# Optimization experiments

Measured on AMD Instinct MI355X. Metric: run time of the kernel, lower is better.

Reference implementation:

```python
import jax, jax.numpy as jnp
import numpy as np

B, S, D = 4, 2048, 1024
NEG = -1e10

def setup_inputs() -> dict:
    key = jax.random.key(0)
    ks = jax.random.split(key, 8)
    scale = 1.0 / np.sqrt(D)
    return {
        "hidden_states": jax.random.normal(ks[0], (B, S, D), jnp.float32),
        "mask": jax.random.randint(ks[1], (B, S), 0, 2, jnp.int32),
        "Wq": jax.random.normal(ks[2], (D, D), jnp.float32) * scale,
        "bq": jnp.zeros((D,), jnp.float32),
        "Wk": jax.random.normal(ks[3], (D, D), jnp.float32) * scale,
        "bk": jnp.zeros((D,), jnp.float32),
        "Wv": jax.random.normal(ks[4], (D, D), jnp.float32) * scale,
        "bv": jnp.zeros((D,), jnp.float32),
        "Wo": jax.random.normal(ks[5], (D, D), jnp.float32) * scale,
        "bo": jnp.zeros((D,), jnp.float32),
    }

def reference(hidden_states, mask, Wq, bq, Wk, bk, Wv, bv, Wo, bo):
    # torch Linear: y = x @ W.T + b
    q = jnp.einsum('bsd,ed->bse', hidden_states, Wq) + bq
    k = jnp.einsum('bsd,ed->bse', hidden_states, Wk) + bk
    v = jnp.einsum('bsd,ed->bse', hidden_states, Wv) + bv
    inv_sqrt_d = jnp.asarray(int(hidden_states.shape[-1]) ** (-0.5), hidden_states.dtype)
    weight = jnp.einsum('bqd,bkd->bqk', q, k) * inv_sqrt_d  # [B,S,S]
    # mask viewed as [B,1,S]: key-padding mask broadcast over query dim
    m = mask.reshape(mask.shape[0], 1, mask.shape[1])
    weight = jnp.where(m == 0, jnp.asarray(NEG, weight.dtype), weight)
    a = jax.nn.softmax(weight, axis=-1)
    hid = jnp.einsum('bqk,bkd->bqd', a, v)
    hid_o = jnp.einsum('bsd,ed->bse', hid, Wo) + bo
    return hidden_states + hid_o  # residual=True
```

## Files before the change

kernel.cpp:

```cpp
#include <hip/hip_runtime.h>
#include <stdint.h>


typedef __attribute__((ext_vector_type(8))) short bf16x8;
typedef __attribute__((ext_vector_type(4))) float f32x4;

typedef __attribute__((address_space(3))) void lds_void_t;
typedef __attribute__((address_space(1))) const void glb_void_t;

__device__ __forceinline__ ushort f2bf(float f) {
  uint32_t u = __float_as_uint(f);
  u += 0x7FFF + ((u >> 16) & 1);
  return (ushort)(u >> 16);
}
__device__ __forceinline__ float bf2f(ushort u) {
  return __uint_as_float(((uint32_t)u) << 16);
}

__global__ __launch_bounds__(256) void convert_all(
    const float* __restrict__ X, const float* __restrict__ Wq,
    const float* __restrict__ Wk, const float* __restrict__ Wv,
    const float* __restrict__ Wo, const float* __restrict__ bq,
    const float* __restrict__ bk, const float* __restrict__ bv,
    ushort* __restrict__ Xb, ushort* __restrict__ Wqkvb,
    ushort* __restrict__ Wob, float* __restrict__ bqkv) {
  if (blockIdx.x >= 12288) {
#pragma unroll
    for (int u = 0; u < 3; ++u) {
      int base = (u * 256 + threadIdx.x) * 4;
      float4 v = (base < 1024)   ? *(const float4*)(bq + base)
               : (base < 2048)   ? *(const float4*)(bk + base - 1024)
                                 : *(const float4*)(bv + base - 2048);
      *(float4*)(bqkv + base) = v;
    }
    return;
  }
  int64_t o4 = ((int64_t)blockIdx.x * blockDim.x + threadIdx.x) * 4;
  const float* s; ushort* d; int64_t doff, soff;
  if (o4 < 8388608)        { s = X;  d = Xb;    doff = o4;            soff = o4; }
  else if (o4 < 9437184)   { s = Wq; d = Wqkvb; doff = o4 - 8388608;  soff = o4 - 8388608; }
  else if (o4 < 10485760)  { s = Wk; d = Wqkvb; doff = o4 - 8388608;  soff = o4 - 9437184; }
  else if (o4 < 11534336)  { s = Wv; d = Wqkvb; doff = o4 - 8388608;  soff = o4 - 10485760; }
  else                     { s = Wo; d = Wob;   doff = o4 - 11534336; soff = o4 - 11534336; }
  float4 v = *(const float4*)(s + soff);
  ushort4 o;
  o.x = f2bf(v.x); o.y = f2bf(v.y); o.z = f2bf(v.z); o.w = f2bf(v.w);
  *(ushort4*)(d + doff) = o;
}

#define BM 128
#define BKT 64

template <int MODE, int BNV, int GM>
__global__ __launch_bounds__(256) void gemm_bt(
    const ushort* __restrict__ Ag, const ushort* __restrict__ Bg,
    void* __restrict__ Og, const float* __restrict__ bias,
    const float* __restrict__ resid, ushort* __restrict__ Vt,
    const int* __restrict__ maskg, float* __restrict__ rowsum,
    int M, int N, int K, int lda, int ldb, int ldo,
    long long sAz, long long sBz, long long sOz, float scale) {
  constexpr int NFR = BNV / 32;
  __shared__ ushort LDSu[BM * BKT + BNV * BKT];
  ushort* const As = LDSu;
  ushort* const Bs = LDSu + BM * BKT;
  __shared__ int redn[4];

  const int z = blockIdx.z;
  const ushort* A = Ag + (int64_t)z * sAz;
  const ushort* B = Bg + (int64_t)z * sBz;

  const int tilesN = N / BNV;
  const int q8 = gridDim.x >> 3;
  const int wg = (blockIdx.x & 7) * q8 + (blockIdx.x >> 3);
  const int grpSz = GM * tilesN;
  const int tm = (wg / grpSz) * GM + (wg % GM);
  const int tn = (wg % grpSz) / GM;
  const int tid = threadIdx.x;
  const int wid = tid >> 6;
  const int lane = tid & 63;
  const int lr = lane & 15;
  const int kq = lane >> 4;
  const int wr = (wid >> 1) * 64;
  const int wc = (wid & 1) * (BNV / 2);

  if constexpr (MODE == 6) {
    const int4* mrow = (const int4*)(maskg + z * 2048);
    int4 ma = mrow[tid * 2];
    int4 mb = mrow[tid * 2 + 1];
    int cnt = (ma.x == 0) + (ma.y == 0) + (ma.z == 0) + (ma.w == 0) +
              (mb.x == 0) + (mb.y == 0) + (mb.z == 0) + (mb.w == 0);
#pragma unroll
    for (int off = 1; off < 64; off <<= 1) cnt += __shfl_xor(cnt, off);
    if (lane == 0) redn[wid] = cnt;
  }

  f32x4 acc[4][NFR];
#pragma unroll
  for (int m = 0; m < 4; ++m)
#pragma unroll
    for (int n = 0; n < NFR; ++n) acc[m][n] = (f32x4){0.f, 0.f, 0.f, 0.f};

  const int64_t abase = (int64_t)tm * BM;
  const int64_t bbase = (int64_t)tn * BNV;

  for (int kt = 0; kt < K; kt += BKT) {
    if (kt) __syncthreads();
#pragma unroll
    for (int r = 0; r < 4; ++r) {
      int idx = r * 256 + tid;
      int row = idx >> 3, slot = idx & 7;
      int sslot = slot ^ (row & 7);
      const ushort* ga = A + (abase + row) * lda + kt + sslot * 8;
      ushort* la = &As[(r * 256 + wid * 64) * 8];
      __builtin_amdgcn_global_load_lds((glb_void_t*)ga, (lds_void_t*)la, 16, 0, 0);
    }
#pragma unroll
    for (int r = 0; r < BNV / 32; ++r) {
      int idx = r * 256 + tid;
      int row = idx >> 3, slot = idx & 7;
      int sslot = slot ^ (row & 7);
      const ushort* gb = B + (bbase + row) * ldb + kt + sslot * 8;
      ushort* lb = &Bs[(r * 256 + wid * 64) * 8];
      __builtin_amdgcn_global_load_lds((glb_void_t*)gb, (lds_void_t*)lb, 16, 0, 0);
    }
    __syncthreads();

#pragma unroll
    for (int kk = 0; kk < 2; ++kk) {
      bf16x8 af[4], bfr[NFR];
#pragma unroll
      for (int m = 0; m < 4; ++m) {
        int row = wr + m * 16 + lr;
        int slot = (kk * 4 + kq) ^ (row & 7);
        af[m] = *(const bf16x8*)&As[row * 64 + slot * 8];
      }
#pragma unroll
      for (int n = 0; n < NFR; ++n) {
        int col = wc + n * 16 + lr;
        int slot = (kk * 4 + kq) ^ (col & 7);
        bfr[n] = *(const bf16x8*)&Bs[col * 64 + slot * 8];
      }
#pragma unroll
      for (int m = 0; m < 4; ++m)
#pragma unroll
        for (int n = 0; n < NFR; ++n)
          acc[m][n] = __builtin_amdgcn_mfma_f32_16x16x32_bf16(af[m], bfr[n], acc[m][n], 0, 0, 0);
    }
  }

  if constexpr (MODE == 5) {
    float part[4][4];
#pragma unroll
    for (int m = 0; m < 4; ++m)
#pragma unroll
      for (int i = 0; i < 4; ++i) part[m][i] = 0.f;
#pragma unroll
    for (int m = 0; m < 4; ++m) {
      int r0 = tm * BM + wr + m * 16 + kq * 4;
#pragma unroll
      for (int n = 0; n < NFR; ++n) {
        int c = tn * BNV + wc + n * 16 + lr;
#pragma unroll
        for (int i = 0; i < 4; ++i) {
          float e = __expf(acc[m][n][i]);
          ((ushort*)Og)[(int64_t)z * sOz + (int64_t)(r0 + i) * ldo + c] = f2bf(e);
          part[m][i] += e;
        }
      }
    }
#pragma unroll
    for (int off = 1; off <= 8; off <<= 1)
#pragma unroll
      for (int m = 0; m < 4; ++m)
#pragma unroll
        for (int i = 0; i < 4; ++i)
          part[m][i] += __shfl_xor(part[m][i], off);
    if (lr == 0) {
#pragma unroll
      for (int m = 0; m < 4; ++m)
#pragma unroll
        for (int i = 0; i < 4; ++i)
          atomicAdd(&rowsum[z * 2048 + tm * BM + wr + m * 16 + kq * 4 + i],
                    part[m][i]);
    }
  } else if constexpr (MODE == 6) {
    float nm = (float)(redn[0] + redn[1] + redn[2] + redn[3]);
    float invr[4][4];
#pragma unroll
    for (int m = 0; m < 4; ++m)
#pragma unroll
      for (int i = 0; i < 4; ++i)
        invr[m][i] =
            1.0f / (rowsum[z * 2048 + tm * BM + wr + m * 16 + kq * 4 + i] - nm);
#pragma unroll
    for (int m = 0; m < 4; ++m) {
      int r0 = tm * BM + wr + m * 16 + kq * 4;
#pragma unroll
      for (int n = 0; n < NFR; ++n) {
        int c = tn * BNV + wc + n * 16 + lr;
#pragma unroll
        for (int i = 0; i < 4; ++i)
          ((ushort*)Og)[(int64_t)z * sOz + (int64_t)(r0 + i) * ldo + c] =
              f2bf(acc[m][n][i] * invr[m][i]);
      }
    }
  } else if constexpr (MODE == 4) {
    if (tn < 8) {
#pragma unroll
      for (int m = 0; m < 4; ++m) {
        int r0 = tm * BM + wr + m * 16 + kq * 4;
#pragma unroll
        for (int n = 0; n < NFR; ++n) {
          int c = tn * BNV + wc + n * 16 + lr;
          const float bb = bias[c];
#pragma unroll
          for (int i = 0; i < 4; ++i)
            ((ushort*)Og)[(int64_t)(r0 + i) * 2048 + c] =
                f2bf((acc[m][n][i] + bb) * 0.03125f);
        }
      }
    } else if (tn < 16) {
#pragma unroll
      for (int m = 0; m < 4; ++m) {
        int r0 = tm * BM + wr + m * 16 + kq * 4;
        int4 mv = *(const int4*)(maskg + r0);
        int mk[4] = {mv.x, mv.y, mv.z, mv.w};
#pragma unroll
        for (int n = 0; n < NFR; ++n) {
          int c = tn * BNV + wc + n * 16 + lr;
          const float bb = bias[c];
#pragma unroll
          for (int i = 0; i < 4; ++i)
            ((ushort*)Og)[(int64_t)(r0 + i) * 2048 + c] =
                mk[i] ? f2bf(acc[m][n][i] + bb) : (ushort)0;
        }
      }
    } else {
      __syncthreads();
#pragma unroll
      for (int m = 0; m < 4; ++m) {
        int rl0 = wr + m * 16 + kq * 4;
        int4 mv = *(const int4*)(maskg + tm * BM + rl0);
        int mk[4] = {mv.x, mv.y, mv.z, mv.w};
#pragma unroll
        for (int n = 0; n < NFR; ++n) {
          int cl = wc + n * 16 + lr;
          const float bb = bias[tn * BNV + cl];
#pragma unroll
          for (int i = 0; i < 4; ++i) {
            int rl = rl0 + i;
            ushort v = mk[i] ? f2bf(acc[m][n][i] + bb) : (ushort)0;
            LDSu[cl * 128 + (rl ^ ((cl & 7) << 3))] = v;
          }
        }
      }
      __syncthreads();
      {
        const int e = tid >> 1, h = tid & 1;
        ushort* dst = Vt + (int64_t)((tn - 16) * BNV + e) * 8192 + tm * BM + h * 64;
        const ushort* src = &LDSu[e * 128 + h * 64];
#pragma unroll
        for (int g = 0; g < 8; ++g) {
          bf16x8 vv = *(const bf16x8*)&src[((g ^ (e & 7)) & 7) * 8];
          *(bf16x8*)&dst[g * 8] = vv;
        }
      }
    }
  } else {
#pragma unroll
    for (int m = 0; m < 4; ++m) {
      int r0 = tm * BM + wr + m * 16 + kq * 4;
#pragma unroll
      for (int n = 0; n < NFR; ++n) {
        int c = tn * BNV + wc + n * 16 + lr;
        const float bb = bias[c];
#pragma unroll
        for (int i = 0; i < 4; ++i) {
          int rrow = r0 + i;
          ((float*)Og)[(int64_t)rrow * ldo + c] =
              acc[m][n][i] + bb + resid[(int64_t)rrow * ldo + c];
        }
      }
    }
  }
}

extern "C" void kernel_launch(void* const* d_in, const int* in_sizes, int n_in,
                              void* d_out, int out_size, void* d_ws, size_t ws_size,
                              hipStream_t stream) {
  const float* hs = (const float*)d_in[0];
  const int* mask = (const int*)d_in[1];
  const float* Wq = (const float*)d_in[2];
  const float* bq = (const float*)d_in[3];
  const float* Wk = (const float*)d_in[4];
  const float* bk = (const float*)d_in[5];
  const float* Wv = (const float*)d_in[6];
  const float* bv = (const float*)d_in[7];
  const float* Wo = (const float*)d_in[8];
  const float* bo = (const float*)d_in[9];
  float* out = (float*)d_out;
  char* w = (char*)d_ws;

  ushort* Xb    = (ushort*)(w + 0);
  float*  rowsum = (float*)(w + 0);
  ushort* Wqkvb = (ushort*)(w + 16777216);
  ushort* Wob   = (ushort*)(w + 23068672);
  ushort* QKb   = (ushort*)(w + 25165824);
  ushort* Vt    = (ushort*)(w + 58720256);
  ushort* P     = (ushort*)(w + 75497472);
  float*  bqkv  = (float*)(w + 92274688);
  ushort* AO    = (ushort*)(w + 109051904);

  convert_all<<<12289, 256, 0, stream>>>(hs, Wq, Wk, Wv, Wo, bq, bk, bv,
                                         Xb, Wqkvb, Wob, bqkv);

  gemm_bt<4, 128, 8><<<dim3(1536, 1, 1), 256, 0, stream>>>(Xb, Wqkvb, QKb, bqkv,
      nullptr, Vt, mask, nullptr,
      8192, 3072, 1024, 1024, 1024, 2048, 0, 0, 0, 1.f);

  hipMemsetAsync(rowsum, 0, 8192 * sizeof(float), stream);

  gemm_bt<5, 128, 8><<<dim3(256, 1, 4), 256, 0, stream>>>(QKb, QKb + 1024, P,
      nullptr, nullptr, nullptr, nullptr, rowsum,
      2048, 2048, 1024, 2048, 2048, 2048,
      (long long)2048 * 2048, (long long)2048 * 2048, (long long)2048 * 2048,
      1.f);

  gemm_bt<6, 128, 4><<<dim3(128, 1, 4), 256, 0, stream>>>(P, Vt, AO, nullptr,
      nullptr, nullptr, mask, rowsum,
      2048, 1024, 2048, 2048, 8192, 1024,
      (long long)2048 * 2048, (long long)2048, (long long)2048 * 1024, 1.f);

  gemm_bt<3, 64, 8><<<dim3(1024, 1, 1), 256, 0, stream>>>(AO, Wob, (void*)out, bo,
      hs, nullptr, nullptr, nullptr,
      8192, 1024, 1024, 1024, 1024, 1024, 0, 0, 0, 1.f);
}
```

Before: 188.2 us.

## Replace scores GEMM with 256x256 tiled 8-wave pipelined kernel

Swaps the generic 128-tile QK^T scores GEMM for a dedicated 512-thread kernel computing 256x256 tiles. It double-buffers direct global-to-LDS loads interleaved with MFMA clusters, using explicit barriers, waitcnts and setprio. It also reduces row sums in LDS before one atomic per row. The aim is more operand reuse, overlap of memory with compute, and fewer atomics, at the cost of heavy LDS use (128KB), fewer blocks (256 total) and fragile hand scheduling.

```diff
diff --git a/kernel.cpp b/kernel.cpp
--- a/kernel.cpp
+++ b/kernel.cpp
@@ -16,6 +16,12 @@
 __device__ __forceinline__ float bf2f(ushort u) {
   return __uint_as_float(((uint32_t)u) << 16);
 }
+
+#define BAR   __builtin_amdgcn_s_barrier()
+#define SCHED __builtin_amdgcn_sched_barrier(0)
+#define LGKM0 asm volatile("s_waitcnt lgkmcnt(0)" ::: "memory")
+#define VMC0  asm volatile("s_waitcnt vmcnt(0)" ::: "memory")
+#define VMC4  asm volatile("s_waitcnt vmcnt(4)" ::: "memory")
 
 __global__ __launch_bounds__(256) void convert_all(
     const float* __restrict__ X, const float* __restrict__ Wq,
@@ -148,42 +154,7 @@
     }
   }
 
-  if constexpr (MODE == 5) {
-    float part[4][4];
-#pragma unroll
-    for (int m = 0; m < 4; ++m)
-#pragma unroll
-      for (int i = 0; i < 4; ++i) part[m][i] = 0.f;
-#pragma unroll
-    for (int m = 0; m < 4; ++m) {
-      int r0 = tm * BM + wr + m * 16 + kq * 4;
-#pragma unroll
-      for (int n = 0; n < NFR; ++n) {
-        int c = tn * BNV + wc + n * 16 + lr;
-#pragma unroll
-        for (int i = 0; i < 4; ++i) {
-          float e = __expf(acc[m][n][i]);
-          ((ushort*)Og)[(int64_t)z * sOz + (int64_t)(r0 + i) * ldo + c] = f2bf(e);
-          part[m][i] += e;
-        }
-      }
-    }
-#pragma unroll
-    for (int off = 1; off <= 8; off <<= 1)
-#pragma unroll
-      for (int m = 0; m < 4; ++m)
-#pragma unroll
-        for (int i = 0; i < 4; ++i)
-          part[m][i] += __shfl_xor(part[m][i], off);
-    if (lr == 0) {
-#pragma unroll
-      for (int m = 0; m < 4; ++m)
-#pragma unroll
-        for (int i = 0; i < 4; ++i)
-          atomicAdd(&rowsum[z * 2048 + tm * BM + wr + m * 16 + kq * 4 + i],
-                    part[m][i]);
-    }
-  } else if constexpr (MODE == 6) {
+  if constexpr (MODE == 6) {
     float nm = (float)(redn[0] + redn[1] + redn[2] + redn[3]);
     float invr[4][4];
 #pragma unroll
@@ -283,6 +254,183 @@
       }
     }
   }
+}
+
+__global__ __launch_bounds__(512, 2) void scores8(
+    const ushort* __restrict__ QKg, ushort* __restrict__ P,
+    float* __restrict__ rowsum) {
+  __shared__ ushort AsU[32768];
+  __shared__ ushort BsU[32768];
+
+  const int z = blockIdx.z;
+  const ushort* Ab = QKg + (int64_t)z * (2048 * 2048);
+  const ushort* Bb = Ab + 1024;
+  const int64_t zoff = (int64_t)z * (2048 * 2048);
+
+  const int q8 = gridDim.x >> 3;
+  const int wg = (blockIdx.x & 7) * q8 + (blockIdx.x >> 3);
+  const int tm = wg >> 3, tn = wg & 7;
+
+  const int tid = threadIdx.x;
+  const int wid = tid >> 6, lane = tid & 63;
+  const int lr = lane & 15, kq = lane >> 4;
+  const int wrh = wid >> 2;
+  const int wcq = wid & 3;
+  const int hB = wcq >> 1;
+  const int wcin = (wcq & 1) * 64;
+
+  const int r0 = tid >> 3;
+  const int g0 = ((tid & 7) ^ (r0 & 7)) * 8;
+  const ushort* gA = Ab + (int64_t)(tm * 256 + r0) * 2048 + g0;
+  const ushort* gB = Bb + (int64_t)(tn * 256 + r0) * 2048 + g0;
+
+#define SGA(BUF, H, KT) do {                                                   \
+    __builtin_amdgcn_global_load_lds(                                          \
+        (glb_void_t*)(gA + (int64_t)((H) * 128) * 2048 + (KT)),                \
+        (lds_void_t*)(AsU + (((BUF) * 2 + (H)) * 1024 + tid) * 8), 16, 0, 0);  \
+    __builtin_amdgcn_global_load_lds(                                          \
+        (glb_void_t*)(gA + (int64_t)((H) * 128 + 64) * 2048 + (KT)),           \
+        (lds_void_t*)(AsU + (((BUF) * 2 + (H)) * 1024 + 512 + tid) * 8), 16, 0, 0); \
+  } while (0)
+#define SGB(BUF, H, KT) do {                                                   \
+    __builtin_amdgcn_global_load_lds(                                          \
+        (glb_void_t*)(gB + (int64_t)((H) * 128) * 2048 + (KT)),                \
+        (lds_void_t*)(BsU + (((BUF) * 2 + (H)) * 1024 + tid) * 8), 16, 0, 0);  \
+    __builtin_amdgcn_global_load_lds(                                          \
+        (glb_void_t*)(gB + (int64_t)((H) * 128 + 64) * 2048 + (KT)),           \
+        (lds_void_t*)(BsU + (((BUF) * 2 + (H)) * 1024 + 512 + tid) * 8), 16, 0, 0); \
+  } while (0)
+
+  const int rsw0 = (kq ^ (lr & 7)) * 8;
+  const int rsw1 = rsw0 ^ 32;
+
+  bf16x8 a[4][2], bb[4][2];
+  f32x4 acc[8][4];
+#pragma unroll
+  for (int m = 0; m < 8; ++m)
+#pragma unroll
+    for (int n = 0; n < 4; ++n) acc[m][n] = (f32x4){0.f, 0.f, 0.f, 0.f};
+
+#define RDA1(BUF, MH, MQ) {                                                    \
+    int rr = ((MH) * 4 + (MQ)) * 16 + lr;                                      \
+    const ushort* p_ = AsU + ((BUF) * 2 + wrh) * 8192 + rr * 64;               \
+    a[MQ][0] = *(const bf16x8*)(p_ + rsw0);                                    \
+    a[MQ][1] = *(const bf16x8*)(p_ + rsw1); }
+#define RDA(BUF, MH) RDA1(BUF, MH, 0) RDA1(BUF, MH, 1) RDA1(BUF, MH, 2) RDA1(BUF, MH, 3)
+#define RDB1(BUF, NH, NQ) {                                                    \
+    int n_ = (NH) * 2 + (NQ);                                                  \
+    int cc = wcin + n_ * 16 + lr;                                              \
+    const ushort* p_ = BsU + ((BUF) * 2 + hB) * 8192 + cc * 64;                \
+    bb[n_][0] = *(const bf16x8*)(p_ + rsw0);                                   \
+    bb[n_][1] = *(const bf16x8*)(p_ + rsw1); }
+#define RDB(BUF, NH) RDB1(BUF, NH, 0) RDB1(BUF, NH, 1)
+#define MM2X(MH, MQ, N) \
+    acc[(MH)*4+(MQ)][N] = __builtin_amdgcn_mfma_f32_16x16x32_bf16(a[MQ][0], bb[N][0], acc[(MH)*4+(MQ)][N], 0, 0, 0); \
+    acc[(MH)*4+(MQ)][N] = __builtin_amdgcn_mfma_f32_16x16x32_bf16(a[MQ][1], bb[N][1], acc[(MH)*4+(MQ)][N], 0, 0, 0);
+#define CL8(MH, NH) \
+    __builtin_amdgcn_s_setprio(1); \
+    MM2X(MH, 0, (NH)*2) MM2X(MH, 0, (NH)*2+1) MM2X(MH, 1, (NH)*2) MM2X(MH, 1, (NH)*2+1) \
+    MM2X(MH, 2, (NH)*2) MM2X(MH, 2, (NH)*2+1) MM2X(MH, 3, (NH)*2) MM2X(MH, 3, (NH)*2+1) \
+    __builtin_amdgcn_s_setprio(0);
+
+  SGA(0, 0, 0); SGA(0, 1, 0); SGB(0, 0, 0); SGB(0, 1, 0);
+  SGB(1, 0, 64); SGB(1, 1, 64);
+  VMC4; BAR; SCHED;
+
+  for (int it = 0; it < 8; ++it) {
+    const bool last = (it == 7);
+    const int ktA1 = it * 128 + 64;
+    const int ktN = it * 128 + 128;
+    const int ktN1 = it * 128 + 192;
+    RDA(0, 0) RDB(0, 0)
+    SGA(1, 0, ktA1);
+    BAR; LGKM0; SCHED;
+    CL8(0, 0)
+    SCHED; BAR;
+    RDB(0, 1)
+    SGA(1, 1, ktA1);
+    BAR; LGKM0; SCHED;
+    CL8(0, 1)
+    SCHED; BAR;
+    RDA(0, 1)
+    if (!last) { SGB(0, 0, ktN); }
+    BAR; LGKM0; SCHED;
+    CL8(1, 1)
+    SCHED; BAR;
+    if (!last) { SGB(0, 1, ktN); }
+    CL8(1, 0)
+    SCHED;
+    if (last) { VMC0; } else { VMC4; }
+    BAR;
+    RDA(1, 0) RDB(1, 0)
+    if (!last) { SGA(0, 0, ktN); }
+    BAR; LGKM0; SCHED;
+    CL8(0, 0)
+    SCHED; BAR;
+    RDB(1, 1)
+    if (!last) { SGA(0, 1, ktN); }
+    BAR; LGKM0; SCHED;
+    CL8(0, 1)
+    SCHED; BAR;
+    RDA(1, 1)
+    if (!last) { SGB(1, 0, ktN1); }
+    BAR; LGKM0; SCHED;
+    CL8(1, 1)
+    SCHED; BAR;
+    if (!last) { SGB(1, 1, ktN1); }
+    CL8(1, 0)
+    SCHED;
+    if (!last) { VMC4; BAR; }
+  }
+
+  float part[8][4];
+#pragma unroll
+  for (int m = 0; m < 8; ++m)
+#pragma unroll
+    for (int i = 0; i < 4; ++i) part[m][i] = 0.f;
+  const int colb = tn * 256 + wcq * 64;
+#pragma unroll
+  for (int m = 0; m < 8; ++m) {
+    const int rl = wrh * 128 + m * 16 + kq * 4;
+#pragma unroll
+    for (int n = 0; n < 4; ++n) {
+      const int c = colb + n * 16 + lr;
+#pragma unroll
+      for (int i = 0; i < 4; ++i) {
+        float e = __expf(acc[m][n][i]);
+        P[zoff + (int64_t)(tm * 256 + rl + i) * 2048 + c] = f2bf(e);
+        part[m][i] += e;
+      }
+    }
+  }
+#pragma unroll
+  for (int off = 1; off <= 8; off <<= 1)
+#pragma unroll
+    for (int m = 0; m < 8; ++m)
+#pragma unroll
+      for (int i = 0; i < 4; ++i)
+        part[m][i] += __shfl_xor(part[m][i], off);
+  float* pbuf = (float*)AsU;
+  if (lr == 0) {
+#pragma unroll
+    for (int m = 0; m < 8; ++m)
+#pragma unroll
+      for (int i = 0; i < 4; ++i)
+        pbuf[wcq * 256 + wrh * 128 + m * 16 + kq * 4 + i] = part[m][i];
+  }
+  __syncthreads();
+  if (tid < 256) {
+    float s = pbuf[tid] + pbuf[256 + tid] + pbuf[512 + tid] + pbuf[768 + tid];
+    atomicAdd(&rowsum[z * 2048 + tm * 256 + tid], s);
+  }
+#undef SGA
+#undef SGB
+#undef RDA1
+#undef RDA
+#undef RDB1
+#undef RDB
+#undef MM2X
+#undef CL8
 }
 
 extern "C" void kernel_launch(void* const* d_in, const int* in_sizes, int n_in,
@@ -320,11 +468,7 @@
 
   hipMemsetAsync(rowsum, 0, 8192 * sizeof(float), stream);
 
-  gemm_bt<5, 128, 8><<<dim3(256, 1, 4), 256, 0, stream>>>(QKb, QKb + 1024, P,
-      nullptr, nullptr, nullptr, nullptr, rowsum,
-      2048, 2048, 1024, 2048, 2048, 2048,
-      (long long)2048 * 2048, (long long)2048 * 2048, (long long)2048 * 2048,
-      1.f);
+  scores8<<<dim3(64, 1, 4), 512, 0, stream>>>(QKb, P, rowsum);
 
   gemm_bt<6, 128, 4><<<dim3(128, 1, 4), 256, 0, stream>>>(P, Vt, AO, nullptr,
       nullptr, nullptr, mask, rowsum,
```

Measured after the change: 177.8 us, median of 2. 1.06x faster.
